# Performance work log

Hardware: AMD Instinct MI355X
Metric: run time of the kernel (lower is better)

Reference implementation:

```python
import jax, jax.numpy as jnp
import numpy as np

D = 1  # dilation


def _unfold3x3(x, d):
    # x: [B, C, H, W] -> [B, H*W, 9, C]; matches torch.nn.Unfold(kernel_size=3,
    # dilation=d, padding=d, stride=1) followed by the module's reshapes.
    B, C, H, W = x.shape
    xp = jnp.pad(x, ((0, 0), (0, 0), (d, d), (d, d)))
    pats = [xp[:, :, i * d:i * d + H, j * d:j * d + W] for i in range(3) for j in range(3)]
    p = jnp.stack(pats, axis=0)  # [9, B, C, H, W], kernel positions row-major (center = 4)
    return p.transpose(1, 3, 4, 0, 2).reshape(B, H * W, 9, C)


def _masked_bn(h, m, gamma, beta, eps=1e-5):
    # BatchNorm1d in training mode applied only to rows selected by bool mask m
    # (the torch code gathers rows, BNs them, scatters back into zeros).
    # Stats are the biased mean/var over the selected rows, per channel.
    axes = tuple(range(h.ndim - 1))
    mf = m[..., None].astype(h.dtype)
    n = jnp.maximum(mf.sum(), 1.0)
    mean = (h * mf).sum(axes) / n
    var = (((h - mean) ** 2 * mf)).sum(axes) / n
    return (h - mean) * jax.lax.rsqrt(var + eps) * gamma + beta


def setup_inputs() -> dict:
    key = jax.random.key(0)
    ks = jax.random.split(key, 8)
    B, H, W = 2, 64, 1024
    Cin, Cout, Cm = 64, 64, 4
    s = 0.1
    x = jax.random.normal(ks[0], (B, Cm + Cin, H, W), jnp.float32)
    mask = (jax.random.uniform(ks[1], (B, 1, H, W)) > 0.3).astype(jnp.float32)
    return {
        "x": x,
        "mask": mask,
        "w1": jax.random.normal(ks[2], (8, Cm), jnp.float32) * s,
        "bn1_g": jnp.ones(8, jnp.float32),
        "bn1_b": jnp.zeros(8, jnp.float32),
        "w2": jax.random.normal(ks[3], (1, 8), jnp.float32) * s,
        "b2": jnp.zeros(1, jnp.float32),
        "g1": jax.random.normal(ks[4], (8, Cm), jnp.float32) * s,
        "gbn1_g": jnp.ones(8, jnp.float32),
        "gbn1_b": jnp.zeros(8, jnp.float32),
        "g2": jax.random.normal(ks[5], (8, 8), jnp.float32) * s,
        "gbn2_g": jnp.ones(8, jnp.float32),
        "gbn2_b": jnp.zeros(8, jnp.float32),
        "w_agg": jax.random.normal(ks[6], (Cout, 72 + Cin), jnp.float32) * s,
        "abn_g": jnp.ones(Cout, jnp.float32),
        "abn_b": jnp.zeros(Cout, jnp.float32),
    }


def reference(x, mask, w1, bn1_g, bn1_b, w2, b2, g1, gbn1_g, gbn1_b, g2, gbn2_g, gbn2_b, w_agg, abn_g, abn_b):
    B, C, H, W = x.shape
    xu = _unfold3x3(x, D)                      # [B, HW, 9, C]
    mu = _unfold3x3(mask, D)[..., 0]           # [B, HW, 9]
    msel = mu > 0                              # valid-neighbor mask
    mp0 = msel[:, :, 4]                        # valid-center mask [B, HW]
    pn = xu[..., :4] - xu[:, :, 4:5, :4]       # relative meta coords [B, HW, 9, 4]
    feats = xu[..., 4:]                        # neighbor features [B, HW, 9, Cin]

    # weight branch (dense compute + mask == torch's gather/scatter)
    h = _masked_bn(pn @ w1.T, msel, bn1_g, bn1_b)
    h = jax.nn.relu(h) @ w2.T + b2             # [B, HW, 9, 1]
    wts = jnp.where(msel, h[..., 0], 0.0)      # zeros at invalid neighbors pre-softmax
    wts = jax.nn.softmax(wts, axis=-1)[..., None]

    fagg = (wts * feats).sum(axis=2)           # [B, HW, Cin]

    # geo branch
    g = jax.nn.relu(_masked_bn(pn @ g1.T, msel, gbn1_g, gbn1_b))
    g = jax.nn.relu(_masked_bn(g @ g2.T, msel, gbn2_g, gbn2_b))
    g = jnp.where(msel[..., None], g, 0.0)
    g = (wts * g).reshape(B, H * W, 72)

    # aggregation over valid centers
    out = jnp.concatenate([fagg, g], axis=-1) @ w_agg.T
    out = jax.nn.relu(_masked_bn(out, mp0, abn_g, abn_b))
    out = jnp.where(mp0[..., None], out, 0.0)  # [B, HW, Cout]
    return out.transpose(0, 2, 1).reshape(B, -1, H, W)  # fold with k=1 == reshape
```

## Files before the change

kernel.cpp:

```cpp
#include <hip/hip_runtime.h>

#define HW_ 65536
#define W_ 1024
#define H_ 64
#define B_ 2
#define C_ 68
#define NPIX 131072
#define EPS 1e-5f

typedef __attribute__((ext_vector_type(8))) short short8;
typedef __attribute__((ext_vector_type(4))) float floatx4;

__device__ __forceinline__ unsigned short f2bf(float f) {
  unsigned u = __float_as_uint(f);
  u += 0x7fffu + ((u >> 16) & 1u);
  return (unsigned short)(u >> 16);
}
__device__ __forceinline__ unsigned pack2(float a, float b) {
  return (unsigned)f2bf(a) | ((unsigned)f2bf(b) << 16);
}
__device__ __forceinline__ float wred(float v) {
  v += __shfl_xor(v, 1);  v += __shfl_xor(v, 2);  v += __shfl_xor(v, 4);
  v += __shfl_xor(v, 8);  v += __shfl_xor(v, 16); v += __shfl_xor(v, 32);
  return v;
}
__device__ __forceinline__ int swz_tile(int bid) {
  return (bid & 7) * 64 + (bid >> 3);
}

__global__ __launch_bounds__(256) void k_stats1(
    const float* __restrict__ x, const float* __restrict__ mask,
    const float* __restrict__ w1, const float* __restrict__ g1,
    float* __restrict__ ws) {
  float acc[34];
#pragma unroll
  for (int i = 0; i < 34; i++) acc[i] = 0.f;

  int p = swz_tile(blockIdx.x) * 256 + threadIdx.x;
  {
    int b = p >> 16, s = p & (HW_ - 1);
    int h = s >> 10, w = s & (W_ - 1);
    const float* xb = x + (size_t)b * C_ * HW_;
    const float* mb = mask + (size_t)b * HW_;
    float xc0 = xb[s], xc1 = xb[HW_ + s], xc2 = xb[2 * HW_ + s], xc3 = xb[3 * HW_ + s];
    acc[33] += (mb[s] > 0.f) ? 1.f : 0.f;
#pragma unroll
    for (int k = 0; k < 9; k++) {
      int di = k / 3 - 1, dj = k % 3 - 1;
      int hh = h + di, ww = w + dj;
      bool inb = ((unsigned)hh < (unsigned)H_) && ((unsigned)ww < (unsigned)W_);
      int ns = hh * W_ + ww;
      float mval = inb ? mb[ns] : 0.f;
      if (mval > 0.f) {
        float pn0 = xb[ns] - xc0;
        float pn1 = xb[HW_ + ns] - xc1;
        float pn2 = xb[2 * HW_ + ns] - xc2;
        float pn3 = xb[3 * HW_ + ns] - xc3;
        acc[32] += 1.f;
#pragma unroll
        for (int o = 0; o < 8; o++) {
          float ta = pn0 * w1[o * 4] + pn1 * w1[o * 4 + 1] + pn2 * w1[o * 4 + 2] + pn3 * w1[o * 4 + 3];
          acc[o] += ta; acc[8 + o] += ta * ta;
          float tg = pn0 * g1[o * 4] + pn1 * g1[o * 4 + 1] + pn2 * g1[o * 4 + 2] + pn3 * g1[o * 4 + 3];
          acc[16 + o] += tg; acc[24 + o] += tg * tg;
        }
      }
    }
  }
  __shared__ float red[4][34];
  int lane = threadIdx.x & 63, wave = threadIdx.x >> 6;
#pragma unroll
  for (int i = 0; i < 34; i++) {
    float r = wred(acc[i]);
    if (lane == 0) red[wave][i] = r;
  }
  __syncthreads();
  if (threadIdx.x < 34)
    atomicAdd(&ws[threadIdx.x],
              red[0][threadIdx.x] + red[1][threadIdx.x] + red[2][threadIdx.x] + red[3][threadIdx.x]);
}

__global__ __launch_bounds__(256) void k_stats2(
    const float* __restrict__ x, const float* __restrict__ mask,
    const float* __restrict__ g1, const float* __restrict__ gbn1_g,
    const float* __restrict__ gbn1_b, const float* __restrict__ g2,
    float* __restrict__ ws) {
  __shared__ float sc[8], sh[8];
  if (threadIdx.x < 8) {
    int o = threadIdx.x;
    float n = fmaxf(ws[32], 1.f);
    float mean = ws[16 + o] / n;
    float var = ws[24 + o] / n - mean * mean;
    float s = gbn1_g[o] * rsqrtf(var + EPS);
    sc[o] = s; sh[o] = gbn1_b[o] - mean * s;
  }
  __syncthreads();

  float acc[16];
#pragma unroll
  for (int i = 0; i < 16; i++) acc[i] = 0.f;

  int p = swz_tile(blockIdx.x) * 256 + threadIdx.x;
  {
    int b = p >> 16, s = p & (HW_ - 1);
    int h = s >> 10, w = s & (W_ - 1);
    const float* xb = x + (size_t)b * C_ * HW_;
    const float* mb = mask + (size_t)b * HW_;
    float xc0 = xb[s], xc1 = xb[HW_ + s], xc2 = xb[2 * HW_ + s], xc3 = xb[3 * HW_ + s];
#pragma unroll
    for (int k = 0; k < 9; k++) {
      int di = k / 3 - 1, dj = k % 3 - 1;
      int hh = h + di, ww = w + dj;
      bool inb = ((unsigned)hh < (unsigned)H_) && ((unsigned)ww < (unsigned)W_);
      int ns = hh * W_ + ww;
      float mval = inb ? mb[ns] : 0.f;
      if (mval > 0.f) {
        float pn0 = xb[ns] - xc0;
        float pn1 = xb[HW_ + ns] - xc1;
        float pn2 = xb[2 * HW_ + ns] - xc2;
        float pn3 = xb[3 * HW_ + ns] - xc3;
        float gb[8];
#pragma unroll
        for (int o = 0; o < 8; o++) {
          float tg = pn0 * g1[o * 4] + pn1 * g1[o * 4 + 1] + pn2 * g1[o * 4 + 2] + pn3 * g1[o * 4 + 3];
          gb[o] = fmaxf(sc[o] * tg + sh[o], 0.f);
        }
#pragma unroll
        for (int j = 0; j < 8; j++) {
          float t2 = 0.f;
#pragma unroll
          for (int o = 0; o < 8; o++) t2 += gb[o] * g2[j * 8 + o];
          acc[j] += t2; acc[8 + j] += t2 * t2;
        }
      }
    }
  }
  __shared__ float red[4][16];
  int lane = threadIdx.x & 63, wave = threadIdx.x >> 6;
#pragma unroll
  for (int i = 0; i < 16; i++) {
    float r = wred(acc[i]);
    if (lane == 0) red[wave][i] = r;
  }
  __syncthreads();
  if (threadIdx.x < 16)
    atomicAdd(&ws[40 + threadIdx.x],
              red[0][threadIdx.x] + red[1][threadIdx.x] + red[2][threadIdx.x] + red[3][threadIdx.x]);
}

__global__ __launch_bounds__(256) void k_fused(
    const float* __restrict__ x, const float* __restrict__ mask,
    const float* __restrict__ w1, const float* __restrict__ bn1_g,
    const float* __restrict__ bn1_b, const float* __restrict__ w2,
    const float* __restrict__ b2, const float* __restrict__ g1,
    const float* __restrict__ gbn1_g, const float* __restrict__ gbn1_b,
    const float* __restrict__ g2, const float* __restrict__ gbn2_g,
    const float* __restrict__ gbn2_b, const float* __restrict__ w_agg,
    const float* __restrict__ ws, float* __restrict__ out_pre,
    float* __restrict__ wsum) {
  __shared__ uint4 vecA[17][256];
  __shared__ float sA[8], hA[8], sG1[8], hG1[8], sG2[8], hG2[8];

  if (threadIdx.x < 24) {
    int o = threadIdx.x & 7;
    float n = fmaxf(ws[32], 1.f);
    float sum, sum2, gma, bta;
    if (threadIdx.x < 8)       { sum = ws[o];      sum2 = ws[8 + o];  gma = bn1_g[o];  bta = bn1_b[o]; }
    else if (threadIdx.x < 16) { sum = ws[16 + o]; sum2 = ws[24 + o]; gma = gbn1_g[o]; bta = gbn1_b[o]; }
    else                       { sum = ws[40 + o]; sum2 = ws[48 + o]; gma = gbn2_g[o]; bta = gbn2_b[o]; }
    float mean = sum / n, var = sum2 / n - mean * mean;
    float s = gma * rsqrtf(var + EPS);
    float sft = bta - mean * s;
    if (threadIdx.x < 8)       { sA[o] = s;  hA[o] = sft; }
    else if (threadIdx.x < 16) { sG1[o] = s; hG1[o] = sft; }
    else                       { sG2[o] = s; hG2[o] = sft; }
  }
  __syncthreads();

  int tile = swz_tile(blockIdx.x);
  int p0 = tile * 256;
  int p = p0 + threadIdx.x;
  int b = p >> 16, s = p & (HW_ - 1);
  int h = s >> 10, w = s & (W_ - 1);
  const float* xb = x + (size_t)b * C_ * HW_;
  const float* mb = mask + (size_t)b * HW_;
  float xc0 = xb[s], xc1 = xb[HW_ + s], xc2 = xb[2 * HW_ + s], xc3 = xb[3 * HW_ + s];
  float b2v = b2[0];

  float ev[9]; int nsv[9]; bool inbv[9], mselv[9];
  float mx = -1e30f;
#pragma unroll
  for (int k = 0; k < 9; k++) {
    int di = k / 3 - 1, dj = k % 3 - 1;
    int hh = h + di, ww = w + dj;
    bool inb = ((unsigned)hh < (unsigned)H_) && ((unsigned)ww < (unsigned)W_);
    int ns = hh * W_ + ww;
    inbv[k] = inb; nsv[k] = ns;
    float mval = inb ? mb[ns] : 0.f;
    bool msel = mval > 0.f;
    mselv[k] = msel;
    float wp = 0.f;
    if (msel) {
      float pn0 = xb[ns] - xc0;
      float pn1 = xb[HW_ + ns] - xc1;
      float pn2 = xb[2 * HW_ + ns] - xc2;
      float pn3 = xb[3 * HW_ + ns] - xc3;
      float accw = 0.f;
#pragma unroll
      for (int o = 0; o < 8; o++) {
        float ta = pn0 * w1[o * 4] + pn1 * w1[o * 4 + 1] + pn2 * w1[o * 4 + 2] + pn3 * w1[o * 4 + 3];
        accw += fmaxf(sA[o] * ta + hA[o], 0.f) * w2[o];
      }
      wp = accw + b2v;
    }
    ev[k] = wp;
    mx = fmaxf(mx, wp);
  }
  float den = 0.f;
#pragma unroll
  for (int k = 0; k < 9; k++) { ev[k] = __expf(ev[k] - mx); den += ev[k]; }
  float inv = 1.f / den;

  float fagg[64];
#pragma unroll
  for (int c = 0; c < 64; c++) fagg[c] = 0.f;

#pragma unroll
  for (int k = 0; k < 9; k++) {
    float wt = ev[k] * inv;
    int ns = nsv[k];
    uint4 pk; pk.x = pk.y = pk.z = pk.w = 0u;
    if (mselv[k]) {
      float pn0 = xb[ns] - xc0;
      float pn1 = xb[HW_ + ns] - xc1;
      float pn2 = xb[2 * HW_ + ns] - xc2;
      float pn3 = xb[3 * HW_ + ns] - xc3;
      float gb[8];
#pragma unroll
      for (int o = 0; o < 8; o++) {
        float tg = pn0 * g1[o * 4] + pn1 * g1[o * 4 + 1] + pn2 * g1[o * 4 + 2] + pn3 * g1[o * 4 + 3];
        gb[o] = fmaxf(sG1[o] * tg + hG1[o], 0.f);
      }
      float gv[8];
#pragma unroll
      for (int j = 0; j < 8; j++) {
        float t2 = 0.f;
#pragma unroll
        for (int o = 0; o < 8; o++) t2 += gb[o] * g2[j * 8 + o];
        float gg = fmaxf(sG2[j] * t2 + hG2[j], 0.f);
        gv[j] = wt * gg;
      }
      pk.x = pack2(gv[0], gv[1]); pk.y = pack2(gv[2], gv[3]);
      pk.z = pack2(gv[4], gv[5]); pk.w = pack2(gv[6], gv[7]);
    }
    vecA[8 + k][threadIdx.x] = pk;
    if (inbv[k]) {
      const float* xf = xb + 4 * HW_ + ns;
#pragma unroll
      for (int c = 0; c < 64; c++) fagg[c] += wt * xf[c * HW_];
    }
  }
#pragma unroll
  for (int c = 0; c < 64; c += 8) {
    uint4 pk;
    pk.x = pack2(fagg[c], fagg[c + 1]);     pk.y = pack2(fagg[c + 2], fagg[c + 3]);
    pk.z = pack2(fagg[c + 4], fagg[c + 5]); pk.w = pack2(fagg[c + 6], fagg[c + 7]);
    vecA[c >> 3][threadIdx.x] = pk;
  }
  __syncthreads();

  int lane = threadIdx.x & 63, wave = threadIdx.x >> 6;
  int q = lane >> 4, r = lane & 15;

  short8 Bf[4][5];
#pragma unroll
  for (int nt = 0; nt < 4; nt++) {
    int n = nt * 16 + r;
#pragma unroll
    for (int ks = 0; ks < 5; ks++) {
      int k0 = ks * 32 + q * 8;
      uint4 pk; pk.x = pk.y = pk.z = pk.w = 0u;
      if (k0 < 136) {
        float4 f0 = *reinterpret_cast<const float4*>(w_agg + n * 136 + k0);
        float4 f1 = *reinterpret_cast<const float4*>(w_agg + n * 136 + k0 + 4);
        pk.x = pack2(f0.x, f0.y); pk.y = pack2(f0.z, f0.w);
        pk.z = pack2(f1.x, f1.y); pk.w = pack2(f1.z, f1.w);
      }
      Bf[nt][ks] = *reinterpret_cast<short8*>(&pk);
    }
  }

  floatx4 acc[4][4];
#pragma unroll
  for (int m = 0; m < 4; m++)
#pragma unroll
    for (int nt = 0; nt < 4; nt++) acc[m][nt] = (floatx4){0.f, 0.f, 0.f, 0.f};

#pragma unroll
  for (int m = 0; m < 4; m++) {
    int mt = wave * 4 + m;
    int pix = mt * 16 + r;
    short8 Af[5];
#pragma unroll
    for (int ks = 0; ks < 5; ks++) {
      int chunk = ks * 4 + q;
      if (chunk < 17)
        Af[ks] = *reinterpret_cast<const short8*>(&vecA[chunk][pix]);
      else
        Af[ks] = (short8){0, 0, 0, 0, 0, 0, 0, 0};
    }
#pragma unroll
    for (int nt = 0; nt < 4; nt++)
#pragma unroll
      for (int ks = 0; ks < 5; ks++)
        acc[m][nt] = __builtin_amdgcn_mfma_f32_16x16x32_bf16(Af[ks], Bf[nt][ks], acc[m][nt], 0, 0, 0);
  }

  float aS[4] = {0.f, 0.f, 0.f, 0.f}, aQ[4] = {0.f, 0.f, 0.f, 0.f};
  int s0 = p0 & (HW_ - 1);
#pragma unroll
  for (int m = 0; m < 4; m++) {
    int mt = wave * 4 + m;
    int srow = s0 + mt * 16 + q * 4;
    float4 mv = *reinterpret_cast<const float4*>(mb + srow);
    float m0 = (mv.x > 0.f) ? 1.f : 0.f, m1 = (mv.y > 0.f) ? 1.f : 0.f;
    float m2 = (mv.z > 0.f) ? 1.f : 0.f, m3 = (mv.w > 0.f) ? 1.f : 0.f;
#pragma unroll
    for (int nt = 0; nt < 4; nt++) {
      int ch = nt * 16 + r;
      float4 ov;
      ov.x = acc[m][nt][0]; ov.y = acc[m][nt][1];
      ov.z = acc[m][nt][2]; ov.w = acc[m][nt][3];
      aS[nt] += ov.x * m0 + ov.y * m1 + ov.z * m2 + ov.w * m3;
      aQ[nt] += ov.x * ov.x * m0 + ov.y * ov.y * m1 + ov.z * ov.z * m2 + ov.w * ov.w * m3;
      *reinterpret_cast<float4*>(out_pre + ((size_t)(b * 64 + ch)) * HW_ + srow) = ov;
    }
  }

  __syncthreads();
  float* rS = (float*)&vecA[0][0];
  float* rQ = rS + 256;
#pragma unroll
  for (int nt = 0; nt < 4; nt++) {
    float v1 = aS[nt], v2 = aQ[nt];
    v1 += __shfl_xor(v1, 16); v1 += __shfl_xor(v1, 32);
    v2 += __shfl_xor(v2, 16); v2 += __shfl_xor(v2, 32);
    if (lane < 16) { rS[wave * 64 + nt * 16 + lane] = v1; rQ[wave * 64 + nt * 16 + lane] = v2; }
  }
  __syncthreads();
  if (threadIdx.x < 64) {
    atomicAdd(&wsum[64 + threadIdx.x],
              rS[threadIdx.x] + rS[64 + threadIdx.x] + rS[128 + threadIdx.x] + rS[192 + threadIdx.x]);
    atomicAdd(&wsum[128 + threadIdx.x],
              rQ[threadIdx.x] + rQ[64 + threadIdx.x] + rQ[128 + threadIdx.x] + rQ[192 + threadIdx.x]);
  }
}

__global__ __launch_bounds__(256) void k_final(
    const float* __restrict__ out_pre, const float* __restrict__ mask,
    const float* __restrict__ abn_g, const float* __restrict__ abn_b,
    const float* __restrict__ ws, float* __restrict__ out) {
  __shared__ float sc[64], sh[64];
  if (threadIdx.x < 64) {
    int c = threadIdx.x;
    float n0 = fmaxf(ws[33], 1.f);
    float mean = ws[64 + c] / n0;
    float var = ws[128 + c] / n0 - mean * mean;
    float s = abn_g[c] * rsqrtf(var + EPS);
    sc[c] = s; sh[c] = abn_b[c] - mean * s;
  }
  __syncthreads();
  int i4 = (blockIdx.x * 256 + threadIdx.x) * 4;
  if (i4 >= B_ * 64 * HW_) return;
  int c = (i4 >> 16) & 63;
  int b = i4 >> 22;
  int s = i4 & (HW_ - 1);
  float4 v = *reinterpret_cast<const float4*>(out_pre + i4);
  float4 m = *reinterpret_cast<const float4*>(mask + (size_t)b * HW_ + s);
  float4 o;
  o.x = (m.x > 0.f) ? fmaxf(v.x * sc[c] + sh[c], 0.f) : 0.f;
  o.y = (m.y > 0.f) ? fmaxf(v.y * sc[c] + sh[c], 0.f) : 0.f;
  o.z = (m.z > 0.f) ? fmaxf(v.z * sc[c] + sh[c], 0.f) : 0.f;
  o.w = (m.w > 0.f) ? fmaxf(v.w * sc[c] + sh[c], 0.f) : 0.f;
  *reinterpret_cast<float4*>(out + i4) = o;
}

extern "C" void kernel_launch(void* const* d_in, const int* in_sizes, int n_in,
                              void* d_out, int out_size, void* d_ws, size_t ws_size,
                              hipStream_t stream) {
  const float* x      = (const float*)d_in[0];
  const float* mask   = (const float*)d_in[1];
  const float* w1     = (const float*)d_in[2];
  const float* bn1_g  = (const float*)d_in[3];
  const float* bn1_b  = (const float*)d_in[4];
  const float* w2     = (const float*)d_in[5];
  const float* b2     = (const float*)d_in[6];
  const float* g1     = (const float*)d_in[7];
  const float* gbn1_g = (const float*)d_in[8];
  const float* gbn1_b = (const float*)d_in[9];
  const float* g2     = (const float*)d_in[10];
  const float* gbn2_g = (const float*)d_in[11];
  const float* gbn2_b = (const float*)d_in[12];
  const float* w_agg  = (const float*)d_in[13];
  const float* abn_g  = (const float*)d_in[14];
  const float* abn_b  = (const float*)d_in[15];
  float* out = (float*)d_out;

  size_t need = 1024 + (size_t)NPIX * 64 * 4;
  if (ws_size < need) return;

  float* wsf = (float*)d_ws;
  float* out_pre = (float*)((char*)d_ws + 1024);

  hipMemsetAsync(d_ws, 0, 1024, stream);
  k_stats1<<<512, 256, 0, stream>>>(x, mask, w1, g1, wsf);
  k_stats2<<<512, 256, 0, stream>>>(x, mask, g1, gbn1_g, gbn1_b, g2, wsf);
  k_fused<<<512, 256, 0, stream>>>(x, mask, w1, bn1_g, bn1_b, w2, b2, g1,
                                   gbn1_g, gbn1_b, g2, gbn2_g, gbn2_b, w_agg,
                                   wsf, out_pre, wsf);
  k_final<<<8192, 256, 0, stream>>>(out_pre, mask, abn_g, abn_b, wsf, out);
}
```

Measured before the change: 224.5 us.

## Split neighbor work across two thread halves in stats and fused kernels

Stats kernels now launch twice as many blocks, each half handling a subset of the 9 neighbor positions, which doubles parallelism on a small grid. The fused kernel uses 512 threads per 256-pixel tile. The two thread halves split neighbor logits, with the softmax exchanged through a shared-memory buffer, and split the 64 feature channels of the weighted aggregation. The MFMA GEMM is re-tiled so 8 waves cover 4 row groups by 2 column groups. This lowers register pressure (fagg goes from 64 to 32 floats) and raises occupancy, at the cost of an extra barrier, more shared memory and redundant center loads.

```diff
diff --git a/kernel.cpp b/kernel.cpp
--- a/kernel.cpp
+++ b/kernel.cpp
@@ -32,38 +32,40 @@
     const float* __restrict__ x, const float* __restrict__ mask,
     const float* __restrict__ w1, const float* __restrict__ g1,
     float* __restrict__ ws) {
+  int half = blockIdx.x >> 9;
+  int p = swz_tile(blockIdx.x & 511) * 256 + threadIdx.x;
+  int b = p >> 16, s = p & (HW_ - 1);
+  int h = s >> 10, w = s & (W_ - 1);
+  const float* xb = x + (size_t)b * C_ * HW_;
+  const float* mb = mask + (size_t)b * HW_;
+  float xc0 = xb[s], xc1 = xb[HW_ + s], xc2 = xb[2 * HW_ + s], xc3 = xb[3 * HW_ + s];
+
   float acc[34];
 #pragma unroll
   for (int i = 0; i < 34; i++) acc[i] = 0.f;
-
-  int p = swz_tile(blockIdx.x) * 256 + threadIdx.x;
-  {
-    int b = p >> 16, s = p & (HW_ - 1);
-    int h = s >> 10, w = s & (W_ - 1);
-    const float* xb = x + (size_t)b * C_ * HW_;
-    const float* mb = mask + (size_t)b * HW_;
-    float xc0 = xb[s], xc1 = xb[HW_ + s], xc2 = xb[2 * HW_ + s], xc3 = xb[3 * HW_ + s];
-    acc[33] += (mb[s] > 0.f) ? 1.f : 0.f;
-#pragma unroll
-    for (int k = 0; k < 9; k++) {
-      int di = k / 3 - 1, dj = k % 3 - 1;
-      int hh = h + di, ww = w + dj;
-      bool inb = ((unsigned)hh < (unsigned)H_) && ((unsigned)ww < (unsigned)W_);
-      int ns = hh * W_ + ww;
-      float mval = inb ? mb[ns] : 0.f;
-      if (mval > 0.f) {
-        float pn0 = xb[ns] - xc0;
-        float pn1 = xb[HW_ + ns] - xc1;
-        float pn2 = xb[2 * HW_ + ns] - xc2;
-        float pn3 = xb[3 * HW_ + ns] - xc3;
-        acc[32] += 1.f;
-#pragma unroll
-        for (int o = 0; o < 8; o++) {
-          float ta = pn0 * w1[o * 4] + pn1 * w1[o * 4 + 1] + pn2 * w1[o * 4 + 2] + pn3 * w1[o * 4 + 3];
-          acc[o] += ta; acc[8 + o] += ta * ta;
-          float tg = pn0 * g1[o * 4] + pn1 * g1[o * 4 + 1] + pn2 * g1[o * 4 + 2] + pn3 * g1[o * 4 + 3];
-          acc[16 + o] += tg; acc[24 + o] += tg * tg;
-        }
+  if (half == 0) acc[33] = (mb[s] > 0.f) ? 1.f : 0.f;
+
+#pragma unroll
+  for (int k = 0; k < 9; k++) {
+    bool mine = (k < 5) ? (half == 0) : (half == 1);
+    if (!mine) continue;
+    int di = k / 3 - 1, dj = k % 3 - 1;
+    int hh = h + di, ww = w + dj;
+    bool inb = ((unsigned)hh < (unsigned)H_) && ((unsigned)ww < (unsigned)W_);
+    int ns = hh * W_ + ww;
+    float mval = inb ? mb[ns] : 0.f;
+    if (mval > 0.f) {
+      float pn0 = xb[ns] - xc0;
+      float pn1 = xb[HW_ + ns] - xc1;
+      float pn2 = xb[2 * HW_ + ns] - xc2;
+      float pn3 = xb[3 * HW_ + ns] - xc3;
+      acc[32] += 1.f;
+#pragma unroll
+      for (int o = 0; o < 8; o++) {
+        float ta = pn0 * w1[o * 4] + pn1 * w1[o * 4 + 1] + pn2 * w1[o * 4 + 2] + pn3 * w1[o * 4 + 3];
+        acc[o] += ta; acc[8 + o] += ta * ta;
+        float tg = pn0 * g1[o * 4] + pn1 * g1[o * 4 + 1] + pn2 * g1[o * 4 + 2] + pn3 * g1[o * 4 + 3];
+        acc[16 + o] += tg; acc[24 + o] += tg * tg;
       }
     }
   }
@@ -71,8 +73,8 @@
   int lane = threadIdx.x & 63, wave = threadIdx.x >> 6;
 #pragma unroll
   for (int i = 0; i < 34; i++) {
-    float r = wred(acc[i]);
-    if (lane == 0) red[wave][i] = r;
+    float rv = wred(acc[i]);
+    if (lane == 0) red[wave][i] = rv;
   }
   __syncthreads();
   if (threadIdx.x < 34)
@@ -91,47 +93,49 @@
     float n = fmaxf(ws[32], 1.f);
     float mean = ws[16 + o] / n;
     float var = ws[24 + o] / n - mean * mean;
-    float s = gbn1_g[o] * rsqrtf(var + EPS);
-    sc[o] = s; sh[o] = gbn1_b[o] - mean * s;
-  }
-  __syncthreads();
-
-  float acc[16];
-#pragma unroll
-  for (int i = 0; i < 16; i++) acc[i] = 0.f;
-
-  int p = swz_tile(blockIdx.x) * 256 + threadIdx.x;
-  {
-    int b = p >> 16, s = p & (HW_ - 1);
-    int h = s >> 10, w = s & (W_ - 1);
-    const float* xb = x + (size_t)b * C_ * HW_;
-    const float* mb = mask + (size_t)b * HW_;
-    float xc0 = xb[s], xc1 = xb[HW_ + s], xc2 = xb[2 * HW_ + s], xc3 = xb[3 * HW_ + s];
-#pragma unroll
-    for (int k = 0; k < 9; k++) {
-      int di = k / 3 - 1, dj = k % 3 - 1;
-      int hh = h + di, ww = w + dj;
-      bool inb = ((unsigned)hh < (unsigned)H_) && ((unsigned)ww < (unsigned)W_);
-      int ns = hh * W_ + ww;
-      float mval = inb ? mb[ns] : 0.f;
-      if (mval > 0.f) {
-        float pn0 = xb[ns] - xc0;
-        float pn1 = xb[HW_ + ns] - xc1;
-        float pn2 = xb[2 * HW_ + ns] - xc2;
-        float pn3 = xb[3 * HW_ + ns] - xc3;
-        float gb[8];
-#pragma unroll
-        for (int o = 0; o < 8; o++) {
-          float tg = pn0 * g1[o * 4] + pn1 * g1[o * 4 + 1] + pn2 * g1[o * 4 + 2] + pn3 * g1[o * 4 + 3];
-          gb[o] = fmaxf(sc[o] * tg + sh[o], 0.f);
-        }
-#pragma unroll
-        for (int j = 0; j < 8; j++) {
-          float t2 = 0.f;
-#pragma unroll
-          for (int o = 0; o < 8; o++) t2 += gb[o] * g2[j * 8 + o];
-          acc[j] += t2; acc[8 + j] += t2 * t2;
-        }
+    float s_ = gbn1_g[o] * rsqrtf(var + EPS);
+    sc[o] = s_; sh[o] = gbn1_b[o] - mean * s_;
+  }
+  __syncthreads();
+
+  int half = blockIdx.x >> 9;
+  int p = swz_tile(blockIdx.x & 511) * 256 + threadIdx.x;
+  int b = p >> 16, s = p & (HW_ - 1);
+  int h = s >> 10, w = s & (W_ - 1);
+  const float* xb = x + (size_t)b * C_ * HW_;
+  const float* mb = mask + (size_t)b * HW_;
+  float xc0 = xb[s], xc1 = xb[HW_ + s], xc2 = xb[2 * HW_ + s], xc3 = xb[3 * HW_ + s];
+
+  float acc2[16];
+#pragma unroll
+  for (int i = 0; i < 16; i++) acc2[i] = 0.f;
+
+#pragma unroll
+  for (int k = 0; k < 9; k++) {
+    bool mine = (k < 5) ? (half == 0) : (half == 1);
+    if (!mine) continue;
+    int di = k / 3 - 1, dj = k % 3 - 1;
+    int hh = h + di, ww = w + dj;
+    bool inb = ((unsigned)hh < (unsigned)H_) && ((unsigned)ww < (unsigned)W_);
+    int ns = hh * W_ + ww;
+    float mval = inb ? mb[ns] : 0.f;
+    if (mval > 0.f) {
+      float pn0 = xb[ns] - xc0;
+      float pn1 = xb[HW_ + ns] - xc1;
+      float pn2 = xb[2 * HW_ + ns] - xc2;
+      float pn3 = xb[3 * HW_ + ns] - xc3;
+      float gb[8];
+#pragma unroll
+      for (int o = 0; o < 8; o++) {
+        float tg = pn0 * g1[o * 4] + pn1 * g1[o * 4 + 1] + pn2 * g1[o * 4 + 2] + pn3 * g1[o * 4 + 3];
+        gb[o] = fmaxf(sc[o] * tg + sh[o], 0.f);
+      }
+#pragma unroll
+      for (int j = 0; j < 8; j++) {
+        float t2 = 0.f;
+#pragma unroll
+        for (int o = 0; o < 8; o++) t2 += gb[o] * g2[j * 8 + o];
+        acc2[j] += t2; acc2[8 + j] += t2 * t2;
       }
     }
   }
@@ -139,8 +143,8 @@
   int lane = threadIdx.x & 63, wave = threadIdx.x >> 6;
 #pragma unroll
   for (int i = 0; i < 16; i++) {
-    float r = wred(acc[i]);
-    if (lane == 0) red[wave][i] = r;
+    float rv = wred(acc2[i]);
+    if (lane == 0) red[wave][i] = rv;
   }
   __syncthreads();
   if (threadIdx.x < 16)
@@ -148,7 +152,7 @@
               red[0][threadIdx.x] + red[1][threadIdx.x] + red[2][threadIdx.x] + red[3][threadIdx.x]);
 }
 
-__global__ __launch_bounds__(256) void k_fused(
+__global__ __launch_bounds__(512, 4) void k_fused(
     const float* __restrict__ x, const float* __restrict__ mask,
     const float* __restrict__ w1, const float* __restrict__ bn1_g,
     const float* __restrict__ bn1_b, const float* __restrict__ w2,
@@ -159,6 +163,7 @@
     const float* __restrict__ ws, float* __restrict__ out_pre,
     float* __restrict__ wsum) {
   __shared__ uint4 vecA[17][256];
+  __shared__ float evb[9][256];
   __shared__ float sA[8], hA[8], sG1[8], hG1[8], sG2[8], hG2[8];
 
   if (threadIdx.x < 24) {
@@ -169,17 +174,20 @@
     else if (threadIdx.x < 16) { sum = ws[16 + o]; sum2 = ws[24 + o]; gma = gbn1_g[o]; bta = gbn1_b[o]; }
     else                       { sum = ws[40 + o]; sum2 = ws[48 + o]; gma = gbn2_g[o]; bta = gbn2_b[o]; }
     float mean = sum / n, var = sum2 / n - mean * mean;
-    float s = gma * rsqrtf(var + EPS);
-    float sft = bta - mean * s;
-    if (threadIdx.x < 8)       { sA[o] = s;  hA[o] = sft; }
-    else if (threadIdx.x < 16) { sG1[o] = s; hG1[o] = sft; }
-    else                       { sG2[o] = s; hG2[o] = sft; }
-  }
-  __syncthreads();
-
+    float s_ = gma * rsqrtf(var + EPS);
+    float sft = bta - mean * s_;
+    if (threadIdx.x < 8)       { sA[o] = s_;  hA[o] = sft; }
+    else if (threadIdx.x < 16) { sG1[o] = s_; hG1[o] = sft; }
+    else                       { sG2[o] = s_; hG2[o] = sft; }
+  }
+  __syncthreads();
+
+  int tid = threadIdx.x;
+  int half = tid >> 8;
+  int pix = tid & 255;
   int tile = swz_tile(blockIdx.x);
   int p0 = tile * 256;
-  int p = p0 + threadIdx.x;
+  int p = p0 + pix;
   int b = p >> 16, s = p & (HW_ - 1);
   int h = s >> 10, w = s & (W_ - 1);
   const float* xb = x + (size_t)b * C_ * HW_;
@@ -187,20 +195,19 @@
   float xc0 = xb[s], xc1 = xb[HW_ + s], xc2 = xb[2 * HW_ + s], xc3 = xb[3 * HW_ + s];
   float b2v = b2[0];
 
-  float ev[9]; int nsv[9]; bool inbv[9], mselv[9];
-  float mx = -1e30f;
+  unsigned mbits = 0u;
 #pragma unroll
   for (int k = 0; k < 9; k++) {
+    bool mine = (k < 5) ? (half == 0) : (half == 1);
+    if (!mine) continue;
     int di = k / 3 - 1, dj = k % 3 - 1;
     int hh = h + di, ww = w + dj;
     bool inb = ((unsigned)hh < (unsigned)H_) && ((unsigned)ww < (unsigned)W_);
     int ns = hh * W_ + ww;
-    inbv[k] = inb; nsv[k] = ns;
     float mval = inb ? mb[ns] : 0.f;
-    bool msel = mval > 0.f;
-    mselv[k] = msel;
     float wp = 0.f;
-    if (msel) {
+    if (mval > 0.f) {
+      mbits |= (1u << k);
       float pn0 = xb[ns] - xc0;
       float pn1 = xb[HW_ + ns] - xc1;
       float pn2 = xb[2 * HW_ + ns] - xc2;
@@ -213,24 +220,28 @@
       }
       wp = accw + b2v;
     }
-    ev[k] = wp;
-    mx = fmaxf(mx, wp);
-  }
+    evb[k][pix] = wp;
+  }
+  __syncthreads();
+
+  float ev[9];
+  float mx = -1e30f;
+#pragma unroll
+  for (int k = 0; k < 9; k++) { ev[k] = evb[k][pix]; mx = fmaxf(mx, ev[k]); }
   float den = 0.f;
 #pragma unroll
   for (int k = 0; k < 9; k++) { ev[k] = __expf(ev[k] - mx); den += ev[k]; }
   float inv = 1.f / den;
 
-  float fagg[64];
-#pragma unroll
-  for (int c = 0; c < 64; c++) fagg[c] = 0.f;
-
 #pragma unroll
   for (int k = 0; k < 9; k++) {
-    float wt = ev[k] * inv;
-    int ns = nsv[k];
+    bool mine = (k < 5) ? (half == 0) : (half == 1);
+    if (!mine) continue;
     uint4 pk; pk.x = pk.y = pk.z = pk.w = 0u;
-    if (mselv[k]) {
+    if ((mbits >> k) & 1u) {
+      int di = k / 3 - 1, dj = k % 3 - 1;
+      int ns = (h + di) * W_ + (w + dj);
+      float wt = ev[k] * inv;
       float pn0 = xb[ns] - xc0;
       float pn1 = xb[HW_ + ns] - xc1;
       float pn2 = xb[2 * HW_ + ns] - xc2;
@@ -253,29 +264,42 @@
       pk.x = pack2(gv[0], gv[1]); pk.y = pack2(gv[2], gv[3]);
       pk.z = pack2(gv[4], gv[5]); pk.w = pack2(gv[6], gv[7]);
     }
-    vecA[8 + k][threadIdx.x] = pk;
-    if (inbv[k]) {
-      const float* xf = xb + 4 * HW_ + ns;
-#pragma unroll
-      for (int c = 0; c < 64; c++) fagg[c] += wt * xf[c * HW_];
-    }
-  }
-#pragma unroll
-  for (int c = 0; c < 64; c += 8) {
+    vecA[8 + k][pix] = pk;
+  }
+
+  float facc[32];
+#pragma unroll
+  for (int c = 0; c < 32; c++) facc[c] = 0.f;
+#pragma unroll
+  for (int k = 0; k < 9; k++) {
+    int di = k / 3 - 1, dj = k % 3 - 1;
+    int hh = h + di, ww = w + dj;
+    bool inb = ((unsigned)hh < (unsigned)H_) && ((unsigned)ww < (unsigned)W_);
+    if (inb) {
+      int ns = hh * W_ + ww;
+      float wt = ev[k] * inv;
+      const float* xf = xb + (size_t)(4 + half * 32) * HW_ + ns;
+#pragma unroll
+      for (int c = 0; c < 32; c++) facc[c] += wt * xf[c * HW_];
+    }
+  }
+#pragma unroll
+  for (int c0 = 0; c0 < 32; c0 += 8) {
     uint4 pk;
-    pk.x = pack2(fagg[c], fagg[c + 1]);     pk.y = pack2(fagg[c + 2], fagg[c + 3]);
-    pk.z = pack2(fagg[c + 4], fagg[c + 5]); pk.w = pack2(fagg[c + 6], fagg[c + 7]);
-    vecA[c >> 3][threadIdx.x] = pk;
-  }
-  __syncthreads();
-
-  int lane = threadIdx.x & 63, wave = threadIdx.x >> 6;
+    pk.x = pack2(facc[c0], facc[c0 + 1]);     pk.y = pack2(facc[c0 + 2], facc[c0 + 3]);
+    pk.z = pack2(facc[c0 + 4], facc[c0 + 5]); pk.w = pack2(facc[c0 + 6], facc[c0 + 7]);
+    vecA[(half * 32 + c0) >> 3][pix] = pk;
+  }
+  __syncthreads();
+
+  int lane = tid & 63, wave = tid >> 6;
   int q = lane >> 4, r = lane & 15;
-
-  short8 Bf[4][5];
-#pragma unroll
-  for (int nt = 0; nt < 4; nt++) {
-    int n = nt * 16 + r;
+  int wr = wave >> 1, wc = wave & 1;
+
+  short8 Bf[2][5];
+#pragma unroll
+  for (int nt = 0; nt < 2; nt++) {
+    int n = wc * 32 + nt * 16 + r;
 #pragma unroll
     for (int ks = 0; ks < 5; ks++) {
       int k0 = ks * 32 + q * 8;
@@ -290,44 +314,43 @@
     }
   }
 
-  floatx4 acc[4][4];
+  floatx4 acc[4][2];
 #pragma unroll
   for (int m = 0; m < 4; m++)
 #pragma unroll
-    for (int nt = 0; nt < 4; nt++) acc[m][nt] = (floatx4){0.f, 0.f, 0.f, 0.f};
+    for (int nt = 0; nt < 2; nt++) acc[m][nt] = (floatx4){0.f, 0.f, 0.f, 0.f};
 
 #pragma unroll
   for (int m = 0; m < 4; m++) {
-    int mt = wave * 4 + m;
-    int pix = mt * 16 + r;
+    int pixm = (wr * 4 + m) * 16 + r;
     short8 Af[5];
 #pragma unroll
     for (int ks = 0; ks < 5; ks++) {
       int chunk = ks * 4 + q;
       if (chunk < 17)
-        Af[ks] = *reinterpret_cast<const short8*>(&vecA[chunk][pix]);
+        Af[ks] = *reinterpret_cast<const short8*>(&vecA[chunk][pixm]);
       else
         Af[ks] = (short8){0, 0, 0, 0, 0, 0, 0, 0};
     }
 #pragma unroll
-    for (int nt = 0; nt < 4; nt++)
+    for (int nt = 0; nt < 2; nt++)
 #pragma unroll
       for (int ks = 0; ks < 5; ks++)
         acc[m][nt] = __builtin_amdgcn_mfma_f32_16x16x32_bf16(Af[ks], Bf[nt][ks], acc[m][nt], 0, 0, 0);
   }
 
-  float aS[4] = {0.f, 0.f, 0.f, 0.f}, aQ[4] = {0.f, 0.f, 0.f, 0.f};
+  float aS[2] = {0.f, 0.f}, aQ[2] = {0.f, 0.f};
   int s0 = p0 & (HW_ - 1);
 #pragma unroll
   for (int m = 0; m < 4; m++) {
-    int mt = wave * 4 + m;
+    int mt = wr * 4 + m;
     int srow = s0 + mt * 16 + q * 4;
     float4 mv = *reinterpret_cast<const float4*>(mb + srow);
     float m0 = (mv.x > 0.f) ? 1.f : 0.f, m1 = (mv.y > 0.f) ? 1.f : 0.f;
     float m2 = (mv.z > 0.f) ? 1.f : 0.f, m3 = (mv.w > 0.f) ? 1.f : 0.f;
 #pragma unroll
-    for (int nt = 0; nt < 4; nt++) {
-      int ch = nt * 16 + r;
+    for (int nt = 0; nt < 2; nt++) {
+      int ch = wc * 32 + nt * 16 + r;
       float4 ov;
       ov.x = acc[m][nt][0]; ov.y = acc[m][nt][1];
       ov.z = acc[m][nt][2]; ov.w = acc[m][nt][3];
@@ -341,18 +364,24 @@
   float* rS = (float*)&vecA[0][0];
   float* rQ = rS + 256;
 #pragma unroll
-  for (int nt = 0; nt < 4; nt++) {
+  for (int nt = 0; nt < 2; nt++) {
     float v1 = aS[nt], v2 = aQ[nt];
     v1 += __shfl_xor(v1, 16); v1 += __shfl_xor(v1, 32);
     v2 += __shfl_xor(v2, 16); v2 += __shfl_xor(v2, 32);
-    if (lane < 16) { rS[wave * 64 + nt * 16 + lane] = v1; rQ[wave * 64 + nt * 16 + lane] = v2; }
-  }
-  __syncthreads();
-  if (threadIdx.x < 64) {
-    atomicAdd(&wsum[64 + threadIdx.x],
-              rS[threadIdx.x] + rS[64 + threadIdx.x] + rS[128 + threadIdx.x] + rS[192 + threadIdx.x]);
-    atomicAdd(&wsum[128 + threadIdx.x],
-              rQ[threadIdx.x] + rQ[64 + threadIdx.x] + rQ[128 + threadIdx.x] + rQ[192 + threadIdx.x]);
+    if (lane < 16) { rS[wave * 32 + nt * 16 + lane] = v1; rQ[wave * 32 + nt * 16 + lane] = v2; }
+  }
+  __syncthreads();
+  if (tid < 64) {
+    int c = tid;
+    int wc_ = c >> 5, nt_ = (c >> 4) & 1, r_ = c & 15;
+    float s1 = 0.f, s2 = 0.f;
+#pragma unroll
+    for (int wr_ = 0; wr_ < 4; wr_++) {
+      int idx = (wr_ * 2 + wc_) * 32 + nt_ * 16 + r_;
+      s1 += rS[idx]; s2 += rQ[idx];
+    }
+    atomicAdd(&wsum[64 + c], s1);
+    atomicAdd(&wsum[128 + c], s2);
   }
 }
 
@@ -366,8 +395,8 @@
     float n0 = fmaxf(ws[33], 1.f);
     float mean = ws[64 + c] / n0;
     float var = ws[128 + c] / n0 - mean * mean;
-    float s = abn_g[c] * rsqrtf(var + EPS);
-    sc[c] = s; sh[c] = abn_b[c] - mean * s;
+    float s_ = abn_g[c] * rsqrtf(var + EPS);
+    sc[c] = s_; sh[c] = abn_b[c] - mean * s_;
   }
   __syncthreads();
   int i4 = (blockIdx.x * 256 + threadIdx.x) * 4;
@@ -413,9 +442,9 @@
   float* out_pre = (float*)((char*)d_ws + 1024);
 
   hipMemsetAsync(d_ws, 0, 1024, stream);
-  k_stats1<<<512, 256, 0, stream>>>(x, mask, w1, g1, wsf);
-  k_stats2<<<512, 256, 0, stream>>>(x, mask, g1, gbn1_g, gbn1_b, g2, wsf);
-  k_fused<<<512, 256, 0, stream>>>(x, mask, w1, bn1_g, bn1_b, w2, b2, g1,
+  k_stats1<<<1024, 256, 0, stream>>>(x, mask, w1, g1, wsf);
+  k_stats2<<<1024, 256, 0, stream>>>(x, mask, g1, gbn1_g, gbn1_b, g2, wsf);
+  k_fused<<<512, 512, 0, stream>>>(x, mask, w1, bn1_g, bn1_b, w2, b2, g1,
                                    gbn1_g, gbn1_b, g2, gbn2_g, gbn2_b, w_agg,
                                    wsf, out_pre, wsf);
   k_final<<<8192, 256, 0, stream>>>(out_pre, mask, abn_g, abn_b, wsf, out);
```

Result: faster. 208.2 us (-7.2%).
